# Kernel tuning notes

Hardware: AMD Instinct MI355X
Metric: run time of the kernel (lower is better)

## Reference

```python
import jax, jax.numpy as jnp
import numpy as np

HEIGHT = 8
WIDTH = 8
C = 3
FEAT = HEIGHT * WIDTH * C  # 192
ENC = 16


def setup_inputs() -> dict:
    key = jax.random.key(0)
    k1, k2, k3, k4, k5 = jax.random.split(key, 5)
    B, H, W = 128, 256, 256
    x = jax.random.normal(k1, (B, C, H, W), dtype=jnp.float32)
    # torch Linear init ~ U(-1/sqrt(fan_in), 1/sqrt(fan_in))
    s1 = 1.0 / np.sqrt(FEAT)
    s2 = 1.0 / np.sqrt(ENC)
    W_enc = jax.random.uniform(k2, (ENC, FEAT), jnp.float32, -s1, s1)
    b_enc = jax.random.uniform(k3, (ENC,), jnp.float32, -s1, s1)
    W_dec = jax.random.uniform(k4, (FEAT, ENC), jnp.float32, -s2, s2)
    b_dec = jax.random.uniform(k5, (FEAT,), jnp.float32, -s2, s2)
    return {"x": x, "W_enc": W_enc, "b_enc": b_enc, "W_dec": W_dec, "b_dec": b_dec}


def reference(x, W_enc, b_enc, W_dec, b_dec):
    B, Cc, H, W = x.shape
    nh, nw = H // HEIGHT, W // WIDTH
    # Extract non-overlapping patches, flattened in (C, h, w) order to match
    # x[:, :, i:i+h, j:j+w].reshape(B, -1) in the original.
    xp = x.reshape(B, Cc, nh, HEIGHT, nw, WIDTH)
    xp = xp.transpose(0, 2, 4, 1, 3, 5).reshape(B, nh, nw, FEAT)  # [B,nh,nw,FEAT]
    h = jax.nn.relu(jnp.einsum('bijf,ef->bije', xp, W_enc) + b_enc)
    out = jax.nn.relu(jnp.einsum('bije,fe->bijf', h, W_dec) + b_dec)
    attention = jax.nn.softmax(out, axis=-1)
    out = attention * out
    # Scatter patches back into image layout.
    y = out.reshape(B, nh, nw, Cc, HEIGHT, WIDTH).transpose(0, 3, 1, 4, 2, 5)
    y = y.reshape(B, Cc, H, W)
    return y
```

## Files before the change

kernel.cpp:

```cpp
#include <hip/hip_runtime.h>
#include <hip/hip_fp16.h>


constexpr int NPATCH = 128 * 32 * 32;
constexpr float L2E  = 1.4426950408889634f;

typedef __fp16 h2 __attribute__((ext_vector_type(2)));

__device__ __forceinline__ float dot2(unsigned int w, h2 xp, float c) {
#if __has_builtin(__builtin_amdgcn_fdot2)
  return __builtin_amdgcn_fdot2(__builtin_bit_cast(h2, w), xp, c, false);
#else
  const h2 wh = __builtin_bit_cast(h2, w);
  return fmaf((float)wh.x, (float)xp.x, fmaf((float)wh.y, (float)xp.y, c));
#endif
}

__global__ void prep_weights(const float* __restrict__ Wenc,
                             const float* __restrict__ Wdec,
                             __half* __restrict__ wenc_h,
                             __half* __restrict__ wdec_h) {
  const int t = blockIdx.x * 512 + threadIdx.x;
  if (t < 3072) {
    wenc_h[t] = __float2half_rn(Wenc[t]);
    wdec_h[t] = __float2half_rn(Wdec[t]);
  }
}

__global__ __launch_bounds__(512, 8) void spatial_attn(
    const float* __restrict__ x,
    const unsigned int* __restrict__ wenc_u,
    const unsigned int* __restrict__ wdec_u,
    const float* __restrict__ benc,
    const float* __restrict__ bdec,
    float* __restrict__ y)
{
  __shared__ float        encl[16 * 512];
  __shared__ unsigned int hlu[8 * 64];
  __shared__ float        sls[512];

  const int tid  = threadIdx.x;
  const int lane = tid & 63;
  const int wv   = __builtin_amdgcn_readfirstlane(tid >> 6);
  const int p    = blockIdx.x * 64 + lane;
  const int b    = p >> 10;
  const int ii   = (p >> 5) & 31;
  const int jj   = p & 31;
  const size_t base = (size_t)b * 196608 + (size_t)ii * 2048 + (size_t)jj * 8;

  unsigned int wdp[3];
  #pragma unroll
  for (int k = 0; k < 3; ++k) wdp[k] = wdec_u[wv * 192 + k * 64 + lane];

  h2 xh[12];
  #pragma unroll
  for (int t = 0; t < 3; ++t) {
    const int cr = 3 * wv + t;
    const float* src = x + base + (cr >> 3) * 65536 + (cr & 7) * 256;
    const float4 v0 = *(const float4*)(src);
    const float4 v1 = *(const float4*)(src + 4);
    xh[t*4+0] = __builtin_amdgcn_cvt_pkrtz(v0.x, v0.y);
    xh[t*4+1] = __builtin_amdgcn_cvt_pkrtz(v0.z, v0.w);
    xh[t*4+2] = __builtin_amdgcn_cvt_pkrtz(v1.x, v1.y);
    xh[t*4+3] = __builtin_amdgcn_cvt_pkrtz(v1.z, v1.w);
  }

  #pragma unroll
  for (int e = 0; e < 16; ++e) {
    const unsigned int* w = wenc_u + e * 96 + wv * 12;
    float a = 0.0f;
    #pragma unroll
    for (int k = 0; k < 12; ++k) a = dot2(w[k], xh[k], a);
    encl[e * 512 + tid] = a;
  }
  __syncthreads();

  {
    const int e0 = 2 * wv;
    const float* c0 = encl + e0 * 512 + lane;
    const float* c1 = c0 + 512;
    float a0 = c0[0], a1 = c1[0];
    #pragma unroll
    for (int w8 = 1; w8 < 8; ++w8) { a0 += c0[w8 * 64]; a1 += c1[w8 * 64]; }
    const h2 hp = __builtin_amdgcn_cvt_pkrtz(fmaxf(a0 + benc[e0],     0.0f),
                                             fmaxf(a1 + benc[e0 + 1], 0.0f));
    hlu[wv * 64 + lane] = __builtin_bit_cast(unsigned int, hp);
  }
  __syncthreads();

  h2 hu[8];
  #pragma unroll
  for (int k = 0; k < 8; ++k)
    hu[k] = __builtin_bit_cast(h2, hlu[k * 64 + lane]);

  float o[24];
  float s = 0.0f;
  #pragma unroll
  for (int q = 0; q < 24; ++q) {
    const int f = wv * 24 + q;
    float v = bdec[f];
    #pragma unroll
    for (int k = 0; k < 8; ++k) {
      const int idx = q * 8 + k;
      const unsigned int wraw =
          __builtin_amdgcn_readlane(wdp[idx >> 6], idx & 63);
      v = dot2(wraw, hu[k], v);
    }
    v = fmaxf(v, 0.0f);
    o[q] = v;
    s += __builtin_amdgcn_exp2f(v * L2E);
  }

  sls[tid] = s;
  __syncthreads();
  float st = sls[lane];
  #pragma unroll
  for (int w8 = 1; w8 < 8; ++w8) st += sls[w8 * 64 + lane];
  const float inv = __builtin_amdgcn_rcpf(st);

  #pragma unroll
  for (int t = 0; t < 3; ++t) {
    const int cr = 3 * wv + t;
    float* dst = y + base + (cr >> 3) * 65536 + (cr & 7) * 256;
    float r[8];
    #pragma unroll
    for (int c = 0; c < 8; ++c) {
      const float ov = o[t * 8 + c];
      r[c] = __builtin_amdgcn_exp2f(ov * L2E) * inv * ov;
    }
    *(float4*)(dst)     = (float4){r[0], r[1], r[2], r[3]};
    *(float4*)(dst + 4) = (float4){r[4], r[5], r[6], r[7]};
  }
}

extern "C" void kernel_launch(void* const* d_in, const int* in_sizes, int n_in,
                              void* d_out, int out_size, void* d_ws, size_t ws_size,
                              hipStream_t stream) {
  const float* x    = (const float*)d_in[0];
  const float* Wenc = (const float*)d_in[1];
  const float* benc = (const float*)d_in[2];
  const float* Wdec = (const float*)d_in[3];
  const float* bdec = (const float*)d_in[4];
  float* y = (float*)d_out;

  __half* wenc_h = (__half*)d_ws;
  __half* wdec_h = wenc_h + 3072;

  hipLaunchKernelGGL(prep_weights, dim3(6), dim3(512), 0, stream,
                     Wenc, Wdec, wenc_h, wdec_h);
  hipLaunchKernelGGL(spatial_attn, dim3(NPATCH / 64), dim3(512), 0, stream,
                     x, (const unsigned int*)wenc_h,
                     (const unsigned int*)wdec_h, benc, bdec, y);
}
```

Before: 191.6 us.

## Map patches to 8-lane groups with DPP reductions and LDS-staged weights

```diff
diff --git a/kernel.cpp b/kernel.cpp
--- a/kernel.cpp
+++ b/kernel.cpp
@@ -16,6 +16,16 @@
 #endif
 }
 
+__device__ __forceinline__ float oct_sum(float v) {
+  v += __int_as_float(__builtin_amdgcn_update_dpp(
+         0, __float_as_int(v), 0x0B1, 0xf, 0xf, true));
+  v += __int_as_float(__builtin_amdgcn_update_dpp(
+         0, __float_as_int(v), 0x04E, 0xf, 0xf, true));
+  v += __int_as_float(__builtin_amdgcn_update_dpp(
+         0, __float_as_int(v), 0x141, 0xf, 0xf, true));
+  return v;
+}
+
 __global__ void prep_weights(const float* __restrict__ Wenc,
                              const float* __restrict__ Wdec,
                              __half* __restrict__ wenc_h,
@@ -27,7 +37,7 @@
   }
 }
 
-__global__ __launch_bounds__(512, 8) void spatial_attn(
+__global__ __launch_bounds__(256, 8) void spatial_attn(
     const float* __restrict__ x,
     const unsigned int* __restrict__ wenc_u,
     const unsigned int* __restrict__ wdec_u,
@@ -35,27 +45,34 @@
     const float* __restrict__ bdec,
     float* __restrict__ y)
 {
-  __shared__ float        encl[16 * 512];
-  __shared__ unsigned int hlu[8 * 64];
-  __shared__ float        sls[512];
+  __shared__ __align__(16) unsigned int wencl[1536];
+  __shared__ __align__(16) unsigned int wdecl[1568];
+  __shared__ __align__(16) float        bdecl[224];
 
   const int tid  = threadIdx.x;
   const int lane = tid & 63;
-  const int wv   = __builtin_amdgcn_readfirstlane(tid >> 6);
-  const int p    = blockIdx.x * 64 + lane;
-  const int b    = p >> 10;
-  const int ii   = (p >> 5) & 31;
-  const int jj   = p & 31;
+  const int wv   = tid >> 6;
+  const int g    = lane >> 3;
+  const int s    = lane & 7;
+
+  #pragma unroll
+  for (int k = 0; k < 6; ++k) {
+    const int i = k * 256 + tid;
+    wencl[i] = wenc_u[i];
+    wdecl[i + (i / 192) * 4] = wdec_u[i];
+  }
+  if (tid < 192) bdecl[(tid / 24) * 28 + (tid % 24)] = bdec[tid];
+
+  const int p  = blockIdx.x * 32 + wv * 8 + g;
+  const int b  = p >> 10;
+  const int ii = (p >> 5) & 31;
+  const int jj = p & 31;
   const size_t base = (size_t)b * 196608 + (size_t)ii * 2048 + (size_t)jj * 8;
-
-  unsigned int wdp[3];
-  #pragma unroll
-  for (int k = 0; k < 3; ++k) wdp[k] = wdec_u[wv * 192 + k * 64 + lane];
 
   h2 xh[12];
   #pragma unroll
   for (int t = 0; t < 3; ++t) {
-    const int cr = 3 * wv + t;
+    const int cr = 3 * s + t;
     const float* src = x + base + (cr >> 3) * 65536 + (cr & 7) * 256;
     const float4 v0 = *(const float4*)(src);
     const float4 v1 = *(const float4*)(src + 4);
@@ -64,63 +81,58 @@
     xh[t*4+2] = __builtin_amdgcn_cvt_pkrtz(v1.x, v1.y);
     xh[t*4+3] = __builtin_amdgcn_cvt_pkrtz(v1.z, v1.w);
   }
+  __syncthreads();
 
+  float h[16];
+  const int we_off = s * 12;
   #pragma unroll
   for (int e = 0; e < 16; ++e) {
-    const unsigned int* w = wenc_u + e * 96 + wv * 12;
+    const uint4 w0 = *(const uint4*)(wencl + e * 96 + we_off);
+    const uint4 w1 = *(const uint4*)(wencl + e * 96 + we_off + 4);
+    const uint4 w2 = *(const uint4*)(wencl + e * 96 + we_off + 8);
     float a = 0.0f;
-    #pragma unroll
-    for (int k = 0; k < 12; ++k) a = dot2(w[k], xh[k], a);
-    encl[e * 512 + tid] = a;
+    a = dot2(w0.x, xh[0], a);  a = dot2(w0.y, xh[1], a);
+    a = dot2(w0.z, xh[2], a);  a = dot2(w0.w, xh[3], a);
+    a = dot2(w1.x, xh[4], a);  a = dot2(w1.y, xh[5], a);
+    a = dot2(w1.z, xh[6], a);  a = dot2(w1.w, xh[7], a);
+    a = dot2(w2.x, xh[8], a);  a = dot2(w2.y, xh[9], a);
+    a = dot2(w2.z, xh[10], a); a = dot2(w2.w, xh[11], a);
+    a = oct_sum(a);
+    h[e] = fmaxf(a + benc[e], 0.0f);
   }
-  __syncthreads();
-
-  {
-    const int e0 = 2 * wv;
-    const float* c0 = encl + e0 * 512 + lane;
-    const float* c1 = c0 + 512;
-    float a0 = c0[0], a1 = c1[0];
-    #pragma unroll
-    for (int w8 = 1; w8 < 8; ++w8) { a0 += c0[w8 * 64]; a1 += c1[w8 * 64]; }
-    const h2 hp = __builtin_amdgcn_cvt_pkrtz(fmaxf(a0 + benc[e0],     0.0f),
-                                             fmaxf(a1 + benc[e0 + 1], 0.0f));
-    hlu[wv * 64 + lane] = __builtin_bit_cast(unsigned int, hp);
-  }
-  __syncthreads();
-
   h2 hu[8];
   #pragma unroll
   for (int k = 0; k < 8; ++k)
-    hu[k] = __builtin_bit_cast(h2, hlu[k * 64 + lane]);
+    hu[k] = __builtin_amdgcn_cvt_pkrtz(h[2*k], h[2*k+1]);
 
   float o[24];
-  float s = 0.0f;
+  #pragma unroll
+  for (int m = 0; m < 6; ++m) {
+    const float4 bv = *(const float4*)(bdecl + s * 28 + 4 * m);
+    o[4*m+0] = bv.x; o[4*m+1] = bv.y; o[4*m+2] = bv.z; o[4*m+3] = bv.w;
+  }
+  float ss = 0.0f;
+  const int wd_off = s * 196;
   #pragma unroll
   for (int q = 0; q < 24; ++q) {
-    const int f = wv * 24 + q;
-    float v = bdec[f];
-    #pragma unroll
-    for (int k = 0; k < 8; ++k) {
-      const int idx = q * 8 + k;
-      const unsigned int wraw =
-          __builtin_amdgcn_readlane(wdp[idx >> 6], idx & 63);
-      v = dot2(wraw, hu[k], v);
-    }
+    const uint4 wa = *(const uint4*)(wdecl + wd_off + q * 8);
+    const uint4 wb = *(const uint4*)(wdecl + wd_off + q * 8 + 4);
+    float v = o[q];
+    v = dot2(wa.x, hu[0], v); v = dot2(wa.y, hu[1], v);
+    v = dot2(wa.z, hu[2], v); v = dot2(wa.w, hu[3], v);
+    v = dot2(wb.x, hu[4], v); v = dot2(wb.y, hu[5], v);
+    v = dot2(wb.z, hu[6], v); v = dot2(wb.w, hu[7], v);
     v = fmaxf(v, 0.0f);
     o[q] = v;
-    s += __builtin_amdgcn_exp2f(v * L2E);
+    ss += __builtin_amdgcn_exp2f(v * L2E);
   }
 
-  sls[tid] = s;
-  __syncthreads();
-  float st = sls[lane];
-  #pragma unroll
-  for (int w8 = 1; w8 < 8; ++w8) st += sls[w8 * 64 + lane];
-  const float inv = __builtin_amdgcn_rcpf(st);
+  ss = oct_sum(ss);
+  const float inv = __builtin_amdgcn_rcpf(ss);
 
   #pragma unroll
   for (int t = 0; t < 3; ++t) {
-    const int cr = 3 * wv + t;
+    const int cr = 3 * s + t;
     float* dst = y + base + (cr >> 3) * 65536 + (cr & 7) * 256;
     float r[8];
     #pragma unroll
@@ -148,7 +160,7 @@
 
   hipLaunchKernelGGL(prep_weights, dim3(6), dim3(512), 0, stream,
                      Wenc, Wdec, wenc_h, wdec_h);
-  hipLaunchKernelGGL(spatial_attn, dim3(NPATCH / 64), dim3(512), 0, stream,
+  hipLaunchKernelGGL(spatial_attn, dim3(NPATCH / 32), dim3(256), 0, stream,
                      x, (const unsigned int*)wenc_h,
                      (const unsigned int*)wdec_h, benc, bdec, y);
 }
```

Result: faster. 187.3 us (-2.3%).
